# Kernel optimization log

Measured on AMD Instinct MI355X. Metric: run time of the kernel, lower is better.

The kernel has to match this reference:

```python
import jax, jax.numpy as jnp
import numpy as np

DIM = 2048; HK = 16; HV = 32; DK = 128; DV = 128; KCONV = 4
EPS = 1e-6; CHUNK = 64
KEY_DIM = HK * DK            # 2048
VALUE_DIM = HV * DV          # 4096
CONV_DIM = 2 * KEY_DIM + VALUE_DIM  # 8192
VR = HV // HK                # 2


def _l2norm(x, eps=1e-6):
    return x * jax.lax.rsqrt(jnp.sum(x * x, -1, keepdims=True) + eps)


def _chunk_gated_delta_rule(q, k, v, g, beta, chunk=CHUNK):
    # q,k: [B,T,H,DK]; v: [B,T,H,DV]; g,beta: [B,T,H]
    B, T, H, Dk = q.shape
    Dv = v.shape[-1]
    N = T // chunk
    q = _l2norm(q) * (Dk ** -0.5)
    k = _l2norm(k)
    rc = lambda t: t.transpose(0, 2, 1, 3).reshape(B, H, N, chunk, t.shape[-1])
    q, k, v = rc(q), rc(k), rc(v)
    g = g.transpose(0, 2, 1).reshape(B, H, N, chunk)
    beta = beta.transpose(0, 2, 1).reshape(B, H, N, chunk)
    v_b = v * beta[..., None]
    k_b = k * beta[..., None]
    g = jnp.cumsum(g, axis=-1)  # intra-chunk cumulative log-decay
    tri = jnp.tril(jnp.ones((chunk, chunk), bool))
    tri_s = jnp.tril(jnp.ones((chunk, chunk), bool), -1)
    diff = g[..., :, None] - g[..., None, :]
    decay = jnp.where(tri, jnp.exp(jnp.where(tri, diff, 0.0)), 0.0)
    # WY representation: T = (I + strict_tril(diag(beta) K K^T decay))^{-1}
    M = jnp.where(tri_s, jnp.einsum('bhnci,bhndi->bhncd', k_b, k) * decay, 0.0)
    eye = jnp.eye(chunk, dtype=q.dtype)
    Tinv = jax.scipy.linalg.solve_triangular(eye + M, jnp.broadcast_to(eye, M.shape), lower=True)
    u = Tinv @ v_b                                  # [B,H,N,C,Dv]
    w = Tinv @ (k_b * jnp.exp(g)[..., None])        # [B,H,N,C,Dk]
    attn_loc = jnp.where(tri, jnp.einsum('bhnci,bhndi->bhncd', q, k) * decay, 0.0)
    qg = q * jnp.exp(g)[..., None]
    g_last = g[..., -1]                             # [B,H,N]
    kdecay = k * jnp.exp(g_last[..., None] - g)[..., None]

    def step(S, inp):  # S: [B,H,Dk,Dv]
        u_i, w_i, a_i, qg_i, kd_i, gl_i = inp
        v_new = u_i - w_i @ S
        o_i = qg_i @ S + a_i @ v_new
        S = S * jnp.exp(gl_i)[..., None, None] + jnp.einsum('bhck,bhcv->bhkv', kd_i, v_new)
        return S, o_i

    S0 = jnp.zeros((B, H, Dk, Dv), q.dtype)
    xs = tuple(jnp.moveaxis(t, 2, 0) for t in (u, w, attn_loc, qg, kdecay, g_last))
    _, o = jax.lax.scan(step, S0, xs)               # [N,B,H,C,Dv]
    return jnp.moveaxis(o, 0, 2).reshape(B, H, T, Dv).transpose(0, 2, 1, 3)


def _forward(x, W_qkvz, W_ba, conv_w, dt_bias, A_log, norm_w, W_out):
    B, T, _ = x.shape
    qkvz = (x @ W_qkvz).reshape(B, T, HK, 2 * DK + 2 * VR * DV)
    ba = (x @ W_ba).reshape(B, T, HK, 2 * VR)
    q, k, v_pre, z_pre = jnp.split(qkvz, [DK, 2 * DK, 2 * DK + VR * DV], axis=3)
    b, a = jnp.split(ba, [VR], axis=3)
    b = b.reshape(B, T, HV)
    a = a.reshape(B, T, HV)
    # mirrors torch: cat -> transpose(1,2) -> reshape(bs,-1,seqlen) (C-order)
    mixed = jnp.concatenate([q, k, v_pre], axis=-1)          # [B,T,HK,512]
    mixed = jnp.transpose(mixed, (0, 2, 1, 3)).reshape(B, -1, T)
    y = jax.lax.conv_general_dilated(
        mixed, conv_w[:, None, :], (1,), [(KCONV - 1, 0)],
        dimension_numbers=('NCH', 'OIH', 'NCH'), feature_group_count=CONV_DIM)
    y = jax.nn.silu(y).transpose(0, 2, 1)                    # [B,T,CONV_DIM]
    q, k, v = jnp.split(y, [KEY_DIM, 2 * KEY_DIM], axis=-1)
    q = q.reshape(B, T, -1, DK)
    k = k.reshape(B, T, -1, DK)
    v = v.reshape(B, T, -1, DV)
    z = z_pre.reshape(B, T, -1, DV)
    beta = jax.nn.sigmoid(b)
    g = -jnp.exp(A_log) * jax.nn.softplus(a + dt_bias)       # [B,T,HV]
    q = jnp.repeat(q, VR, axis=2)
    k = jnp.repeat(k, VR, axis=2)
    o = _chunk_gated_delta_rule(q, k, v, g, beta)            # [B,T,HV,DV]
    # FusedRMSNormGated: gate (silu) before RMS norm
    og = o * jax.nn.silu(z)
    og = og * jax.lax.rsqrt(jnp.mean(og * og, -1, keepdims=True) + EPS) * norm_w
    return og.reshape(B, T, -1) @ W_out


def setup_inputs() -> dict:
    key = jax.random.key(0)
    ks = jax.random.split(key, 8)
    B, T = 1, 4096
    x = jax.random.normal(ks[0], (B, T, DIM), jnp.float32)
    rope_cache = jax.random.normal(ks[1], (T, DK), jnp.float32)
    position_ids = jnp.broadcast_to(jnp.arange(T, dtype=jnp.int32)[None, :], (B, T))
    W_qkvz = jax.random.normal(ks[2], (DIM, 2 * KEY_DIM + 2 * VALUE_DIM), jnp.float32) * (DIM ** -0.5)
    W_ba = jax.random.normal(ks[3], (DIM, 2 * HV), jnp.float32) * (DIM ** -0.5)
    conv_w = jax.random.normal(ks[4], (CONV_DIM, KCONV), jnp.float32) * 0.3
    dt_bias = jnp.ones((HV,), jnp.float32)
    A_log = jnp.log(jax.random.uniform(ks[5], (HV,), jnp.float32, 0.05, 4.0))
    norm_w = jnp.ones((DV,), jnp.float32)
    W_out = jax.random.normal(ks[6], (VALUE_DIM, DIM), jnp.float32) * (VALUE_DIM ** -0.5)
    return {"x": x, "rope_cache": rope_cache, "position_ids": position_ids,
            "W_qkvz": W_qkvz, "W_ba": W_ba, "conv_w": conv_w, "dt_bias": dt_bias,
            "A_log": A_log, "norm_w": norm_w, "W_out": W_out}


def reference(x, rope_cache, position_ids, W_qkvz, W_ba, conv_w, dt_bias, A_log, norm_w, W_out):
    # rope_cache / position_ids are accepted but unused, as in the torch module.
    return _forward(x, W_qkvz, W_ba, conv_w, dt_bias, A_log, norm_w, W_out)
```

## Files before the change

### kernel.cpp

```cpp
#include <hip/hip_runtime.h>
#include <hip/hip_bf16.h>

#define NH_K 16
#define NH_V 32
#define D_K 128
#define D_V 128
#define QKVZ_COLS 12288

typedef __attribute__((ext_vector_type(8))) __bf16 bf16x8;
typedef __attribute__((ext_vector_type(4))) __bf16 bf16x4;
typedef __attribute__((ext_vector_type(2))) __bf16 bf16x2;
typedef __attribute__((ext_vector_type(4))) float floatx4;
typedef __attribute__((ext_vector_type(4))) unsigned int uint32x4;

#define GLDS16(gp, lp) __builtin_amdgcn_global_load_lds( \
    (const __attribute__((address_space(1))) unsigned int*)(gp), \
    (__attribute__((address_space(3))) unsigned int*)(lp), 16, 0, 0)

__device__ __forceinline__ float sigm(float x) {
  float e = expf(-fabsf(x));
  return (x >= 0.f) ? 1.f / (1.f + e) : e / (1.f + e);
}
__device__ __forceinline__ float clampf(float v, float m) {
  return fminf(fmaxf(v, -m), m);
}
__device__ __forceinline__ float loadF(const void* p, size_t i, bool f32) {
  return f32 ? ((const float*)p)[i] : (float)((const __bf16*)p)[i];
}

__global__ __launch_bounds__(256) void detect_kernel(
    const unsigned int* __restrict__ x, int* __restrict__ flag)
{
  __shared__ int cnt;
  if (threadIdx.x == 0) cnt = 0;
  __syncthreads();
  unsigned int w = x[threadIdx.x];
  int e = (w >> 7) & 0xFF;
  if (e >= 100 && e <= 135) atomicAdd(&cnt, 1);
  __syncthreads();
  if (threadIdx.x == 0) *flag = (cnt < 128) ? 1 : 0;
}

__global__ __launch_bounds__(256) void convx_kernel(
    const void* __restrict__ x, __bf16* __restrict__ xb,
    const int* __restrict__ flagp)
{
  const bool f32 = (*flagp != 0);
  size_t i = ((size_t)blockIdx.x * 256 + threadIdx.x) * 8;
  if (f32) {
    float4 a = *(const float4*)&((const float*)x)[i];
    float4 b = *(const float4*)&((const float*)x)[i + 4];
    bf16x8 v;
    v[0]=(__bf16)a.x; v[1]=(__bf16)a.y; v[2]=(__bf16)a.z; v[3]=(__bf16)a.w;
    v[4]=(__bf16)b.x; v[5]=(__bf16)b.y; v[6]=(__bf16)b.z; v[7]=(__bf16)b.w;
    *(bf16x8*)&xb[i] = v;
  } else {
    *(uint32x4*)&xb[i] = *(const uint32x4*)&((const __bf16*)x)[i];
  }
}

__global__ __launch_bounds__(256) void trans_kernel(
    const void* __restrict__ W, __bf16* __restrict__ WT,
    int K, int N, const int* __restrict__ flagp)
{
  const bool f32 = (*flagp != 0);
  __shared__ float t[32][33];
  const int k0 = blockIdx.x * 32, n0 = blockIdx.y * 32;
  const int tid = threadIdx.x;
  {
    int r = tid >> 3, c4 = (tid & 7) * 4;
    if (f32) {
      float4 v = *(const float4*)&((const float*)W)[(size_t)(k0 + r) * N + n0 + c4];
      t[r][c4] = v.x; t[r][c4 + 1] = v.y; t[r][c4 + 2] = v.z; t[r][c4 + 3] = v.w;
    } else {
      bf16x4 v = *(const bf16x4*)&((const __bf16*)W)[(size_t)(k0 + r) * N + n0 + c4];
      t[r][c4] = (float)v[0]; t[r][c4 + 1] = (float)v[1];
      t[r][c4 + 2] = (float)v[2]; t[r][c4 + 3] = (float)v[3];
    }
  }
  __syncthreads();
  {
    int n = tid >> 3, k4 = (tid & 7) * 4;
    bf16x4 o;
#pragma unroll
    for (int j = 0; j < 4; ++j) o[j] = (__bf16)t[k4 + j][n];
    *(bf16x4*)&WT[(size_t)(n0 + n) * K + k0 + k4] = o;
  }
}

template<bool OUT_F32>
__global__ __launch_bounds__(512, 1) void gemm_bt2(
    const __bf16* __restrict__ A, const __bf16* __restrict__ BT,
    void* __restrict__ C, int M, int N, int K)
{
  __shared__ __align__(16) __bf16 As[2][8192];
  __shared__ __align__(16) __bf16 Bs[2][8192];
  const int tid = threadIdx.x;
  const int nx  = gridDim.x;
  const int nwg = nx * gridDim.y;
  int lid = blockIdx.y * nx + blockIdx.x;
  int swz = (lid & 7) * (nwg >> 3) + (lid >> 3);
  const int bn = (swz % nx) * 256;
  const int bm = (swz / nx) * 256;
  const int lane = tid & 63;
  const int wv   = tid >> 6;
  const int wm2  = wv >> 2;
  const int wn2  = wv & 3;
  const int l15  = lane & 15;
  const int quad = lane >> 4;
  const int NT   = K >> 5;

  auto stage = [&](int kt, int slot) {
    const int k0 = kt * 32;
#pragma unroll
    for (int L = 0; L < 2; ++L) {
      const int boff = L * 8192 + wv * 1024 + lane * 16;
      const int swb  = boff ^ (((boff >> 9) & 1) << 5);
      const int row  = swb >> 6;
      const int ce   = (swb & 63) >> 1;
      GLDS16(&A[(size_t)(bm + row) * K + k0 + ce], &As[slot][L * 4096 + wv * 512]);
      GLDS16(&BT[(size_t)(bn + row) * K + k0 + ce], &Bs[slot][L * 4096 + wv * 512]);
    }
  };

  floatx4 acc[8][4];
#pragma unroll
  for (int a = 0; a < 8; ++a)
#pragma unroll
    for (int b = 0; b < 4; ++b)
      acc[a][b] = (floatx4){0.f, 0.f, 0.f, 0.f};

  const int flip  = (l15 & 8) ? 32 : 0;
  const int baseA = (((wm2 * 128 + l15) * 64 + quad * 16) ^ flip);
  const int baseB = (((wn2 * 64 + l15) * 64 + quad * 16) ^ flip);

  stage(0, 0);
  stage(1, 1);
  asm volatile("s_waitcnt vmcnt(4)" ::: "memory");
  __builtin_amdgcn_s_barrier();
  __builtin_amdgcn_sched_barrier(0);

  for (int kt = 0; kt < NT; ++kt) {
    const int cur = kt & 1;
    const char* Ab = (const char*)&As[cur][0];
    const char* Bb = (const char*)&Bs[cur][0];
    bf16x8 af[8], bfr[4];
#pragma unroll
    for (int mt = 0; mt < 8; ++mt)
      af[mt] = *(const bf16x8*)(Ab + baseA + mt * 1024);
#pragma unroll
    for (int nt = 0; nt < 4; ++nt)
      bfr[nt] = *(const bf16x8*)(Bb + baseB + nt * 1024);
#pragma unroll
    for (int mt = 0; mt < 8; ++mt)
#pragma unroll
      for (int nt = 0; nt < 4; ++nt)
        acc[mt][nt] = __builtin_amdgcn_mfma_f32_16x16x32_bf16(af[mt], bfr[nt], acc[mt][nt], 0, 0, 0);
    if (kt + 1 < NT) {
      __builtin_amdgcn_s_barrier();
      if (kt + 2 < NT) {
        stage(kt + 2, cur);
        asm volatile("s_waitcnt vmcnt(4)" ::: "memory");
      } else {
        asm volatile("s_waitcnt vmcnt(0)" ::: "memory");
      }
      __builtin_amdgcn_s_barrier();
      __builtin_amdgcn_sched_barrier(0);
    }
  }

#pragma unroll
  for (int mt = 0; mt < 8; ++mt)
#pragma unroll
    for (int nt = 0; nt < 4; ++nt)
#pragma unroll
      for (int r = 0; r < 4; ++r) {
        int row = bm + wm2 * 128 + mt * 16 + quad * 4 + r;
        int col = bn + wn2 * 64 + nt * 16 + l15;
        if (OUT_F32) ((float*)C)[(size_t)row * N + col] = acc[mt][nt][r];
        else         ((__bf16*)C)[(size_t)row * N + col] = (__bf16)acc[mt][nt][r];
      }
}

__global__ __launch_bounds__(64) void ba_kernel(
    const void* __restrict__ x, const void* __restrict__ Wba,
    float* __restrict__ ba, const int* __restrict__ flagp)
{
  __shared__ float xr[2048];
  const bool f32 = (*flagp != 0);
  int t = blockIdx.x, tid = threadIdx.x;
  for (int i = tid; i < 2048; i += 64) xr[i] = loadF(x, (size_t)t * 2048 + i, f32);
  __syncthreads();
  float acc = 0.f;
  for (int k = 0; k < 2048; ++k) acc += xr[k] * loadF(Wba, (size_t)k * 64 + tid, f32);
  ba[(size_t)t * 64 + tid] = acc;
}

__global__ __launch_bounds__(256) void conv_kernel(
    const __bf16* __restrict__ qkvz, const void* __restrict__ conv_w,
    __bf16* __restrict__ qn, __bf16* __restrict__ kn, __bf16* __restrict__ vv,
    const int* __restrict__ flagp)
{
  __shared__ __bf16 yin[128][266];
  const bool f32 = (*flagp != 0);
  const int slot = blockIdx.x;
  const int tb   = blockIdx.y;
  const int tid  = threadIdx.x;
  int kind, h_out, cbase;
  if (slot < 16)      { kind = 0; h_out = slot;      cbase = slot * 128; }
  else if (slot < 32) { kind = 1; h_out = slot - 16; cbase = 2048 + h_out * 128; }
  else                { kind = 2; h_out = slot - 32; cbase = 4096 + h_out * 128; }
  const int hc  = cbase >> 9;
  const int cl0 = cbase & 511;
  const int t0  = tb * 256;

  for (int ch = tid; ch < 128 * 33; ch += 256) {
    int d = ch / 33, k = ch - d * 33;
    int s2 = t0 - 8 + k * 8;
    uint32x4 val;
    if (s2 < 0) {
      val = (uint32x4){0u, 0u, 0u, 0u};
    } else {
      int p  = (cl0 + d) * 4096 + s2;
      int tp = p >> 9, ep = p & 511;
      val = *(const uint32x4*)&qkvz[(size_t)tp * QKVZ_COLS + hc * 768 + ep];
    }
    unsigned int* dst = (unsigned int*)&yin[d][k * 8];
    dst[0] = val[0]; dst[1] = val[1]; dst[2] = val[2]; dst[3] = val[3];
  }
  __syncthreads();

  const int wv   = tid >> 6;
  const int lane = tid & 63;
  float w0[4], w1[4];
#pragma unroll
  for (int j = 0; j < 4; ++j) {
    w0[j] = loadF(conv_w, (size_t)(cbase + lane) * 4 + j, f32);
    w1[j] = loadF(conv_w, (size_t)(cbase + lane + 64) * 4 + j, f32);
  }
  const int ltend = wv * 64 + 64;
  for (int lt = wv * 64; lt < ltend; ++lt) {
    int t = t0 + lt;
    float a0 = 0.f, a1 = 0.f;
#pragma unroll
    for (int j = 0; j < 4; ++j) {
      a0 += w0[j] * (float)yin[lane][lt + 5 + j];
      a1 += w1[j] * (float)yin[lane + 64][lt + 5 + j];
    }
    float v0 = a0 * sigm(a0), v1 = a1 * sigm(a1);
    if (kind == 2) {
      vv[((size_t)t * NH_V + h_out) * D_V + lane]      = (__bf16)v0;
      vv[((size_t)t * NH_V + h_out) * D_V + lane + 64] = (__bf16)v1;
    } else {
      float ss = v0 * v0 + v1 * v1;
#pragma unroll
      for (int off = 32; off; off >>= 1) ss += __shfl_xor(ss, off, 64);
      float scl = rsqrtf(ss + 1e-6f);
      if (kind == 0) scl *= 0.08838834764831845f;
      __bf16* dst = (kind == 0) ? qn : kn;
      dst[((size_t)t * NH_K + h_out) * D_K + lane]      = (__bf16)(v0 * scl);
      dst[((size_t)t * NH_K + h_out) * D_K + lane + 64] = (__bf16)(v1 * scl);
    }
  }
}

__global__ __launch_bounds__(64) void gb_kernel(
    const float* __restrict__ ba, const void* __restrict__ dt_bias,
    const void* __restrict__ A_log, float* __restrict__ gbuf,
    float* __restrict__ betabuf, const int* __restrict__ flagp)
{
  const bool f32 = (*flagp != 0);
  int t = blockIdx.x;
  int hv = threadIdx.x;
  if (hv >= 32) return;
  float bv = ba[t * 64 + (hv >> 1) * 4 + (hv & 1)];
  float av = ba[t * 64 + (hv >> 1) * 4 + 2 + (hv & 1)];
  float beta = sigm(bv);
  float xx = av + loadF(dt_bias, hv, f32);
  float sp = (xx > 15.f) ? xx : log1pf(expf(fminf(xx, 15.f)));
  float g = -expf(loadF(A_log, hv, f32)) * sp;
  gbuf[t * 32 + hv] = g;
  betabuf[t * 32 + hv] = beta;
}

__global__ __launch_bounds__(256) void prep_kernel(
    const __bf16* __restrict__ qn, const __bf16* __restrict__ kn, const __bf16* __restrict__ vv,
    const float* __restrict__ gbuf, const float* __restrict__ betabuf,
    float* __restrict__ gcs, __bf16* __restrict__ u, __bf16* __restrict__ w,
    __bf16* __restrict__ attn)
{
  __shared__ float MT[64][67];
  __shared__ __bf16 vT[128][72];
  __shared__ __bf16 kT[128][72];
  __shared__ float gc[64], betas[64], scu[64], scw[64];
  const int bid = blockIdx.x;
  const int hv = bid >> 6, n = bid & 63;
  const int hk = hv >> 1;
  const int t0 = n * 64;
  const int tid = threadIdx.x;
  const int wv = tid >> 6, lane = tid & 63;
  const int l15 = lane & 15, quad = lane >> 4;

  {
    const __bf16* vrow = &vv[((size_t)(t0 + lane) * NH_V + hv) * D_V + wv * 32];
    const __bf16* krow = &kn[((size_t)(t0 + lane) * NH_K + hk) * D_K + wv * 32];
#pragma unroll
    for (int c2 = 0; c2 < 4; ++c2) {
      bf16x8 v8 = *(const bf16x8*)&vrow[c2 * 8];
      bf16x8 k8 = *(const bf16x8*)&krow[c2 * 8];
#pragma unroll
      for (int j = 0; j < 8; ++j) {
        vT[wv * 32 + c2 * 8 + j][lane] = v8[j];
        kT[wv * 32 + c2 * 8 + j][lane] = k8[j];
      }
    }
  }
  if (tid < 64) {
    gc[tid]    = gbuf[(t0 + tid) * 32 + hv];
    betas[tid] = betabuf[(t0 + tid) * 32 + hv];
  }
  __syncthreads();
  if (tid == 0) {
    float s = 0.f;
    for (int i = 0; i < 64; ++i) { s += gc[i]; gc[i] = s; }
  }
  __syncthreads();
  if (tid < 64) {
    float g = gc[tid];
    gcs[((size_t)hv * 64 + n) * 64 + tid] = g;
    scu[tid] = betas[tid];
    scw[tid] = betas[tid] * expf(g);
  }

  floatx4 kk[4];
#pragma unroll
  for (int nt = 0; nt < 4; ++nt) kk[nt] = (floatx4){0.f, 0.f, 0.f, 0.f};
#pragma unroll
  for (int ks = 0; ks < 4; ++ks) {
    bf16x8 afr = *(const bf16x8*)&kn[((size_t)(t0 + wv * 16 + l15) * NH_K + hk) * D_K + ks * 32 + quad * 8];
#pragma unroll
    for (int nt = 0; nt < 4; ++nt) {
      bf16x8 bfr = *(const bf16x8*)&kn[((size_t)(t0 + nt * 16 + l15) * NH_K + hk) * D_K + ks * 32 + quad * 8];
      kk[nt] = __builtin_amdgcn_mfma_f32_16x16x32_bf16(afr, bfr, kk[nt], 0, 0, 0);
    }
  }
#pragma unroll
  for (int nt = 0; nt < 4; ++nt)
#pragma unroll
    for (int r = 0; r < 4; ++r) {
      int i = wv * 16 + quad * 4 + r;
      int j = nt * 16 + l15;
      float m = 0.f;
      if (j < i) m = kk[nt][r] * betas[i] * expf(fminf(gc[i] - gc[j], 0.f));
      MT[i][j] = m;
    }
  __syncthreads();

  if (wv == 0) {
    if (lane == 0) MT[0][0] = 1.f;
    for (int ii = 1; ii < 64; ++ii) {
      float s = 0.f;
      for (int l = 0; l < ii; ++l) s += MT[ii][l] * MT[l][lane];
      MT[ii][lane] = ((lane == ii) ? 1.f : 0.f) - s;
    }
  }
  {
    int band = (wv == 0) ? 3 : (wv - 1);
    floatx4 at[4];
#pragma unroll
    for (int nt = 0; nt < 4; ++nt) at[nt] = (floatx4){0.f, 0.f, 0.f, 0.f};
#pragma unroll
    for (int ks = 0; ks < 4; ++ks) {
      bf16x8 afr = *(const bf16x8*)&qn[((size_t)(t0 + band * 16 + l15) * NH_K + hk) * D_K + ks * 32 + quad * 8];
#pragma unroll
      for (int nt = 0; nt < 4; ++nt) {
        bf16x8 bfr = *(const bf16x8*)&kn[((size_t)(t0 + nt * 16 + l15) * NH_K + hk) * D_K + ks * 32 + quad * 8];
        at[nt] = __builtin_amdgcn_mfma_f32_16x16x32_bf16(afr, bfr, at[nt], 0, 0, 0);
      }
    }
    size_t abase = ((size_t)hv * 64 + n) * (64 * 64);
#pragma unroll
    for (int nt = 0; nt < 4; ++nt)
#pragma unroll
      for (int r = 0; r < 4; ++r) {
        int i = band * 16 + quad * 4 + r;
        int j = nt * 16 + l15;
        float dec = expf(fminf(gc[i] - gc[j], 0.f));
        float a = (j <= i) ? clampf(at[nt][r] * dec, 1e6f) : 0.f;
        attn[abase + (size_t)i * 64 + j] = (__bf16)a;
      }
  }
  __syncthreads();

  floatx4 ua[8], wa[8];
#pragma unroll
  for (int t = 0; t < 8; ++t) {
    ua[t] = (floatx4){0.f, 0.f, 0.f, 0.f};
    wa[t] = (floatx4){0.f, 0.f, 0.f, 0.f};
  }
#pragma unroll
  for (int ks = 0; ks < 2; ++ks) {
    bf16x8 uh, ul, wh, wl;
#pragma unroll
    for (int j = 0; j < 8; ++j) {
      int c = ks * 32 + quad * 8 + j;
      float raw = MT[wv * 16 + l15][c];
      float tu = raw * scu[c];
      float tw = raw * scw[c];
      __bf16 h1 = (__bf16)tu; uh[j] = h1; ul[j] = (__bf16)(tu - (float)h1);
      __bf16 h2 = (__bf16)tw; wh[j] = h2; wl[j] = (__bf16)(tw - (float)h2);
    }
#pragma unroll
    for (int nt = 0; nt < 8; ++nt) {
      bf16x8 vb = *(const bf16x8*)&vT[nt * 16 + l15][ks * 32 + quad * 8];
      ua[nt] = __builtin_amdgcn_mfma_f32_16x16x32_bf16(uh, vb, ua[nt], 0, 0, 0);
      ua[nt] = __builtin_amdgcn_mfma_f32_16x16x32_bf16(ul, vb, ua[nt], 0, 0, 0);
      bf16x8 kb = *(const bf16x8*)&kT[nt * 16 + l15][ks * 32 + quad * 8];
      wa[nt] = __builtin_amdgcn_mfma_f32_16x16x32_bf16(wh, kb, wa[nt], 0, 0, 0);
      wa[nt] = __builtin_amdgcn_mfma_f32_16x16x32_bf16(wl, kb, wa[nt], 0, 0, 0);
    }
  }
  size_t base = ((size_t)hv * 64 + n) * (64 * 128);
#pragma unroll
  for (int nt = 0; nt < 8; ++nt)
#pragma unroll
    for (int r = 0; r < 4; ++r) {
      int row = wv * 16 + quad * 4 + r;
      int dv  = nt * 16 + l15;
      u[base + (size_t)row * 128 + dv] = (__bf16)clampf(ua[nt][r], 1e6f);
      w[base + (size_t)row * 128 + dv] = (__bf16)clampf(wa[nt][r], 1e6f);
    }
}

__global__ __launch_bounds__(64, 1) void scan_kernel(
    const __bf16* __restrict__ u, const __bf16* __restrict__ w, const __bf16* __restrict__ attn,
    const __bf16* __restrict__ qn, const __bf16* __restrict__ kn, const float* __restrict__ gcs,
    __bf16* __restrict__ obuf)
{
  __shared__ __bf16 sb_hi[16][136];
  __shared__ __bf16 sb_lo[16][136];
  __shared__ __bf16 vt[16][72];
  __shared__ __bf16 kt[128][72];

  const int hv   = blockIdx.x & 31;
  const int band = blockIdx.x >> 5;
  const int dv0  = band * 16;
  const int hk   = hv >> 1;
  const int lane = threadIdx.x;
  const int l15  = lane & 15;
  const int quad = lane >> 4;

  floatx4 S[8];
#pragma unroll
  for (int m = 0; m < 8; ++m) S[m] = (floatx4){0.f, 0.f, 0.f, 0.f};
  for (int i = lane; i < 16 * 136 / 2; i += 64) {
    ((unsigned int*)sb_hi)[i] = 0u;
    ((unsigned int*)sb_lo)[i] = 0u;
  }

  for (int n = 0; n < 64; ++n) {
    const int t0 = n * 64;
    const size_t cb = (size_t)hv * 64 + n;
    const float* gr = gcs + cb * 64;
    const size_t ub = cb * 8192;

    const __bf16* krow = &kn[((size_t)(t0 + lane) * NH_K + hk) * D_K];
    bf16x8 kr[16];
#pragma unroll
    for (int c2 = 0; c2 < 16; ++c2) kr[c2] = *(const bf16x8*)&krow[c2 * 8];

    floatx4 av[4];
#pragma unroll
    for (int mt = 0; mt < 4; ++mt)
#pragma unroll
      for (int r = 0; r < 4; ++r)
        av[mt][r] = (float)u[ub + (size_t)(mt * 16 + quad * 4 + r) * 128 + dv0 + l15];

    bf16x8 sh[4], sl[4];
#pragma unroll
    for (int ks = 0; ks < 4; ++ks) {
      sh[ks] = *(const bf16x8*)&sb_hi[l15][ks * 32 + quad * 8];
      sl[ks] = *(const bf16x8*)&sb_lo[l15][ks * 32 + quad * 8];
    }

#pragma unroll
    for (int ks = 0; ks < 4; ++ks)
#pragma unroll
      for (int mt = 0; mt < 4; ++mt) {
        uint32x4 wu = *(const uint32x4*)&w[ub + (size_t)(mt * 16 + l15) * 128 + ks * 32 + quad * 8];
        wu[0] ^= 0x80008000u; wu[1] ^= 0x80008000u;
        wu[2] ^= 0x80008000u; wu[3] ^= 0x80008000u;
        bf16x8 wf = __builtin_bit_cast(bf16x8, wu);
        av[mt] = __builtin_amdgcn_mfma_f32_16x16x32_bf16(wf, sh[ks], av[mt], 0, 0, 0);
        av[mt] = __builtin_amdgcn_mfma_f32_16x16x32_bf16(wf, sl[ks], av[mt], 0, 0, 0);
      }
#pragma unroll
    for (int mt = 0; mt < 4; ++mt) {
      bf16x4 h4;
#pragma unroll
      for (int r = 0; r < 4; ++r) h4[r] = (__bf16)clampf(av[mt][r], 1e8f);
      *(bf16x4*)&vt[l15][mt * 16 + quad * 4] = h4;
    }

    const float gl  = gr[63];
    const float egl = expf(gl);
    float egr[16];
#pragma unroll
    for (int mt = 0; mt < 4; ++mt)
#pragma unroll
      for (int r = 0; r < 4; ++r)
        egr[mt * 4 + r] = expf(gr[mt * 16 + quad * 4 + r]);
    float ek0[8], ek1[8];
#pragma unroll
    for (int j = 0; j < 8; ++j) {
      ek0[j] = expf(fminf(gl - gr[quad * 8 + j], 0.f));
      ek1[j] = expf(fminf(gl - gr[32 + quad * 8 + j], 0.f));
    }

    floatx4 ao[4];
#pragma unroll
    for (int mt = 0; mt < 4; ++mt) ao[mt] = (floatx4){0.f, 0.f, 0.f, 0.f};
#pragma unroll
    for (int ks = 0; ks < 4; ++ks)
#pragma unroll
      for (int mt = 0; mt < 4; ++mt) {
        bf16x8 qf = *(const bf16x8*)&qn[((size_t)(t0 + mt * 16 + l15) * NH_K + hk) * D_K + ks * 32 + quad * 8];
        ao[mt] = __builtin_amdgcn_mfma_f32_16x16x32_bf16(qf, sh[ks], ao[mt], 0, 0, 0);
        ao[mt] = __builtin_amdgcn_mfma_f32_16x16x32_bf16(qf, sl[ks], ao[mt], 0, 0, 0);
      }
#pragma unroll
    for (int mt = 0; mt < 4; ++mt)
#pragma unroll
      for (int r = 0; r < 4; ++r) ao[mt][r] *= egr[mt * 4 + r];

#pragma unroll
    for (int c2 = 0; c2 < 16; ++c2)
#pragma unroll
      for (int j = 0; j < 8; ++j)
        kt[c2 * 8 + j][lane] = kr[c2][j];

    bf16x8 vf0 = *(const bf16x8*)&vt[l15][quad * 8];
    bf16x8 vf1 = *(const bf16x8*)&vt[l15][32 + quad * 8];
#pragma unroll
    for (int mt = 0; mt < 4; ++mt) {
      bf16x8 a0 = *(const bf16x8*)&attn[cb * 4096 + (size_t)(mt * 16 + l15) * 64 + quad * 8];
      bf16x8 a1 = *(const bf16x8*)&attn[cb * 4096 + (size_t)(mt * 16 + l15) * 64 + 32 + quad * 8];
      ao[mt] = __builtin_amdgcn_mfma_f32_16x16x32_bf16(a0, vf0, ao[mt], 0, 0, 0);
      ao[mt] = __builtin_amdgcn_mfma_f32_16x16x32_bf16(a1, vf1, ao[mt], 0, 0, 0);
    }
#pragma unroll
    for (int mt = 0; mt < 4; ++mt)
#pragma unroll
      for (int r = 0; r < 4; ++r)
        obuf[((size_t)(t0 + mt * 16 + quad * 4 + r) * NH_V + hv) * D_V + dv0 + l15]
            = (__bf16)clampf(ao[mt][r], 1e8f);

#pragma unroll
    for (int m = 0; m < 8; ++m)
#pragma unroll
      for (int r = 0; r < 4; ++r) S[m][r] *= egl;
    bf16x8 vfd0, vfd1;
#pragma unroll
    for (int j = 0; j < 8; ++j) {
      vfd0[j] = (__bf16)((float)vf0[j] * ek0[j]);
      vfd1[j] = (__bf16)((float)vf1[j] * ek1[j]);
    }
#pragma unroll
    for (int ks = 0; ks < 2; ++ks) {
      bf16x8 vf = ks ? vfd1 : vfd0;
#pragma unroll
      for (int m = 0; m < 8; ++m) {
        bf16x8 kf = *(const bf16x8*)&kt[m * 16 + l15][ks * 32 + quad * 8];
        S[m] = __builtin_amdgcn_mfma_f32_16x16x32_bf16(kf, vf, S[m], 0, 0, 0);
      }
    }
#pragma unroll
    for (int m = 0; m < 8; ++m) {
      bf16x4 h4, l4;
#pragma unroll
      for (int r = 0; r < 4; ++r) {
        float v = clampf(S[m][r], 1e8f);
        S[m][r] = v;
        __bf16 h = (__bf16)v;
        h4[r] = h;
        l4[r] = (__bf16)(v - (float)h);
      }
      *(bf16x4*)&sb_hi[l15][m * 16 + quad * 4] = h4;
      *(bf16x4*)&sb_lo[l15][m * 16 + quad * 4] = l4;
    }
  }
}

__global__ __launch_bounds__(256) void gate_kernel(
    const __bf16* __restrict__ obuf, const __bf16* __restrict__ qkvz,
    const void* __restrict__ norm_w, __bf16* __restrict__ og,
    const int* __restrict__ flagp)
{
  const bool f32 = (*flagp != 0);
  const int t = blockIdx.x;
  const int wv = threadIdx.x >> 6, lane = threadIdx.x & 63;
  const int hv = blockIdx.y * 4 + wv;
  const int d = lane * 2;
  bf16x2 ov = *(const bf16x2*)&obuf[((size_t)t * NH_V + hv) * D_V + d];
  bf16x2 zv = *(const bf16x2*)&qkvz[(size_t)t * QKVZ_COLS + (hv >> 1) * 768 + 512 + (hv & 1) * 128 + d];
  float z0 = (float)zv[0], z1 = (float)zv[1];
  float v0 = (float)ov[0] * (z0 * sigm(z0));
  float v1 = (float)ov[1] * (z1 * sigm(z1));
  float ss = v0 * v0 + v1 * v1;
#pragma unroll
  for (int off = 32; off; off >>= 1) ss += __shfl_xor(ss, off, 64);
  float scl = rsqrtf(ss * (1.f / 128.f) + 1e-6f);
  bf16x2 o;
  o[0] = (__bf16)(v0 * scl * loadF(norm_w, d, f32));
  o[1] = (__bf16)(v1 * scl * loadF(norm_w, d + 1, f32));
  *(bf16x2*)&og[(size_t)t * 4096 + hv * 128 + d] = o;
}

extern "C" void kernel_launch(void* const* d_in, const int* in_sizes, int n_in,
                              void* d_out, int out_size, void* d_ws, size_t ws_size,
                              hipStream_t stream) {
  (void)in_sizes; (void)n_in; (void)out_size;
  const void* x     = d_in[0];
  const void* Wqkvz = d_in[3];
  const void* Wba   = d_in[4];
  const void* convw = d_in[5];
  const void* dtb   = d_in[6];
  const void* Alog  = d_in[7];
  const void* normw = d_in[8];
  const void* Wout  = d_in[9];

  char* ws = (char*)d_ws;
  size_t off = 0;
  int*    flag = (int*)(ws + off);    off += 256;
  __bf16* qkvz = (__bf16*)(ws + off); off += (size_t)4096 * 12288 * 2;
  float* ba    = (float*)(ws + off);  off += (size_t)4096 * 64 * 4;
  float* gbuf  = (float*)(ws + off);  off += (size_t)4096 * 32 * 4;
  float* betab = (float*)(ws + off);  off += (size_t)4096 * 32 * 4;
  float* gcs   = (float*)(ws + off);  off += (size_t)32 * 64 * 64 * 4;
  __bf16* qn   = (__bf16*)(ws + off); off += (size_t)4096 * 2048 * 2;
  __bf16* kn   = (__bf16*)(ws + off); off += (size_t)4096 * 2048 * 2;
  __bf16* vv   = (__bf16*)(ws + off); off += (size_t)4096 * 4096 * 2;
  __bf16* ubuf = (__bf16*)(ws + off); off += (size_t)32 * 64 * 8192 * 2;
  __bf16* wbuf = (__bf16*)(ws + off); off += (size_t)32 * 64 * 8192 * 2;
  __bf16* attn = (__bf16*)(ws + off); off += (size_t)32 * 64 * 4096 * 2;
  __bf16* obuf = vv;
  __bf16* og   = ubuf;
  __bf16* WqkvzT = ubuf;
  __bf16* xb     = attn;
  __bf16* WoutT  = wbuf;
  if (ws_size < off) return;

  detect_kernel<<<1, 256, 0, stream>>>((const unsigned int*)x, flag);
  convx_kernel<<<4096, 256, 0, stream>>>(x, xb, flag);
  trans_kernel<<<dim3(64, 384), 256, 0, stream>>>(Wqkvz, WqkvzT, 2048, 12288, flag);
  gemm_bt2<false><<<dim3(48, 16), 512, 0, stream>>>(xb, WqkvzT, qkvz, 4096, 12288, 2048);
  ba_kernel<<<4096, 64, 0, stream>>>(x, Wba, ba, flag);
  conv_kernel<<<dim3(64, 16), 256, 0, stream>>>(qkvz, convw, qn, kn, vv, flag);
  gb_kernel<<<4096, 64, 0, stream>>>(ba, dtb, Alog, gbuf, betab, flag);
  prep_kernel<<<2048, 256, 0, stream>>>(qn, kn, vv, gbuf, betab, gcs, ubuf, wbuf, attn);
  scan_kernel<<<256, 64, 0, stream>>>(ubuf, wbuf, attn, qn, kn, gcs, obuf);
  gate_kernel<<<dim3(4096, 8), 256, 0, stream>>>(obuf, qkvz, normw, og, flag);
  trans_kernel<<<dim3(128, 64), 256, 0, stream>>>(Wout, WoutT, 4096, 2048, flag);
  gemm_bt2<true><<<dim3(8, 16), 512, 0, stream>>>(og, WoutT, d_out, 4096, 2048, 4096);
}
```

Measured before the change: 1.486 ms.

## Split scan across four waves with LDS reduction; use 128-tile GEMM for output

The recurrent scan kernel now runs 256 threads per block instead of 64. Each wave handles a 32-wide K slice of the state for the w@S and q@S products, the four partial sums are reduced through shared memory, and each wave owns two of the eight state tiles for the update. This shortens the serial per-chunk critical path and spreads state registers across waves, at the cost of extra barriers and LDS traffic. The output projection moves to a new 128x128-tile GEMM with 512 blocks instead of 128 large-tile blocks, which should fill more compute units but has no double buffering.

```diff
diff --git a/kernel.cpp b/kernel.cpp
--- a/kernel.cpp
+++ b/kernel.cpp
@@ -86,6 +86,78 @@
     for (int j = 0; j < 4; ++j) o[j] = (__bf16)t[k4 + j][n];
     *(bf16x4*)&WT[(size_t)(n0 + n) * K + k0 + k4] = o;
   }
+}
+
+template<bool OUT_F32>
+__global__ __launch_bounds__(256) void gemm_bt(
+    const __bf16* __restrict__ A, const __bf16* __restrict__ BT,
+    void* __restrict__ C, int M, int N, int K)
+{
+  __shared__ __align__(16) __bf16 As[128 * 32];
+  __shared__ __align__(16) __bf16 Bs[128 * 32];
+  const int tid = threadIdx.x;
+  const int nx  = gridDim.x;
+  const int nwg = nx * gridDim.y;
+  int lid = blockIdx.y * nx + blockIdx.x;
+  int swz = (lid & 7) * (nwg >> 3) + (lid >> 3);
+  const int bn = (swz % nx) * 128;
+  const int bm = (swz / nx) * 128;
+  const int lane = tid & 63;
+  const int wv   = tid >> 6;
+  const int wm   = (wv >> 1) * 64;
+  const int wn   = (wv & 1) * 64;
+  const int l15  = lane & 15;
+  const int quad = lane >> 4;
+
+  const int o0 = wv * 2048 + lane * 16;
+  const int o1 = o0 + 1024;
+  const __bf16* Ag0 = &A[(size_t)(bm + (o0 >> 6)) * K + ((o0 & 63) >> 1)];
+  const __bf16* Ag1 = &A[(size_t)(bm + (o1 >> 6)) * K + ((o1 & 63) >> 1)];
+  const __bf16* Bg0 = &BT[(size_t)(bn + (o0 >> 6)) * K + ((o0 & 63) >> 1)];
+  const __bf16* Bg1 = &BT[(size_t)(bn + (o1 >> 6)) * K + ((o1 & 63) >> 1)];
+  __bf16* Ad0 = &As[wv * 1024];
+  __bf16* Ad1 = &As[wv * 1024 + 512];
+  __bf16* Bd0 = &Bs[wv * 1024];
+  __bf16* Bd1 = &Bs[wv * 1024 + 512];
+
+  floatx4 acc[4][4];
+#pragma unroll
+  for (int a = 0; a < 4; ++a)
+#pragma unroll
+    for (int b = 0; b < 4; ++b)
+      acc[a][b] = (floatx4){0.f, 0.f, 0.f, 0.f};
+
+  for (int k0 = 0; k0 < K; k0 += 32) {
+    GLDS16(Ag0 + k0, Ad0);
+    GLDS16(Ag1 + k0, Ad1);
+    GLDS16(Bg0 + k0, Bd0);
+    GLDS16(Bg1 + k0, Bd1);
+    __syncthreads();
+    bf16x8 af[4], bfr[4];
+#pragma unroll
+    for (int mt = 0; mt < 4; ++mt)
+      af[mt] = *(const bf16x8*)&As[(wm + mt * 16 + l15) * 32 + quad * 8];
+#pragma unroll
+    for (int nt = 0; nt < 4; ++nt)
+      bfr[nt] = *(const bf16x8*)&Bs[(wn + nt * 16 + l15) * 32 + quad * 8];
+#pragma unroll
+    for (int mt = 0; mt < 4; ++mt)
+#pragma unroll
+      for (int nt = 0; nt < 4; ++nt)
+        acc[mt][nt] = __builtin_amdgcn_mfma_f32_16x16x32_bf16(af[mt], bfr[nt], acc[mt][nt], 0, 0, 0);
+    __syncthreads();
+  }
+#pragma unroll
+  for (int mt = 0; mt < 4; ++mt)
+#pragma unroll
+    for (int nt = 0; nt < 4; ++nt)
+#pragma unroll
+      for (int r = 0; r < 4; ++r) {
+        int row = bm + wm + mt * 16 + quad * 4 + r;
+        int col = bn + wn + nt * 16 + l15;
+        if (OUT_F32) ((float*)C)[(size_t)row * N + col] = acc[mt][nt][r];
+        else         ((__bf16*)C)[(size_t)row * N + col] = (__bf16)acc[mt][nt][r];
+      }
 }
 
 template<bool OUT_F32>
@@ -432,7 +504,7 @@
     }
 }
 
-__global__ __launch_bounds__(64, 1) void scan_kernel(
+__global__ __launch_bounds__(256, 1) void scan_kernel(
     const __bf16* __restrict__ u, const __bf16* __restrict__ w, const __bf16* __restrict__ attn,
     const __bf16* __restrict__ qn, const __bf16* __restrict__ kn, const float* __restrict__ gcs,
     __bf16* __restrict__ obuf)
@@ -441,22 +513,27 @@
   __shared__ __bf16 sb_lo[16][136];
   __shared__ __bf16 vt[16][72];
   __shared__ __bf16 kt[128][72];
+  __shared__ float redv[4][4][64][4];
+  __shared__ float redo[4][4][64][4];
 
   const int hv   = blockIdx.x & 31;
   const int band = blockIdx.x >> 5;
   const int dv0  = band * 16;
   const int hk   = hv >> 1;
-  const int lane = threadIdx.x;
+  const int tid  = threadIdx.x;
+  const int wv   = tid >> 6;
+  const int lane = tid & 63;
   const int l15  = lane & 15;
   const int quad = lane >> 4;
 
-  floatx4 S[8];
-#pragma unroll
-  for (int m = 0; m < 8; ++m) S[m] = (floatx4){0.f, 0.f, 0.f, 0.f};
-  for (int i = lane; i < 16 * 136 / 2; i += 64) {
+  floatx4 S[2];
+  S[0] = (floatx4){0.f, 0.f, 0.f, 0.f};
+  S[1] = (floatx4){0.f, 0.f, 0.f, 0.f};
+  for (int i = tid; i < 16 * 136 / 2; i += 256) {
     ((unsigned int*)sb_hi)[i] = 0u;
     ((unsigned int*)sb_lo)[i] = 0u;
   }
+  __syncthreads();
 
   for (int n = 0; n < 64; ++n) {
     const int t0 = n * 64;
@@ -464,101 +541,94 @@
     const float* gr = gcs + cb * 64;
     const size_t ub = cb * 8192;
 
-    const __bf16* krow = &kn[((size_t)(t0 + lane) * NH_K + hk) * D_K];
-    bf16x8 kr[16];
-#pragma unroll
-    for (int c2 = 0; c2 < 16; ++c2) kr[c2] = *(const bf16x8*)&krow[c2 * 8];
-
-    floatx4 av[4];
-#pragma unroll
-    for (int mt = 0; mt < 4; ++mt)
-#pragma unroll
-      for (int r = 0; r < 4; ++r)
-        av[mt][r] = (float)u[ub + (size_t)(mt * 16 + quad * 4 + r) * 128 + dv0 + l15];
-
-    bf16x8 sh[4], sl[4];
-#pragma unroll
-    for (int ks = 0; ks < 4; ++ks) {
-      sh[ks] = *(const bf16x8*)&sb_hi[l15][ks * 32 + quad * 8];
-      sl[ks] = *(const bf16x8*)&sb_lo[l15][ks * 32 + quad * 8];
-    }
-
-#pragma unroll
-    for (int ks = 0; ks < 4; ++ks)
-#pragma unroll
-      for (int mt = 0; mt < 4; ++mt) {
-        uint32x4 wu = *(const uint32x4*)&w[ub + (size_t)(mt * 16 + l15) * 128 + ks * 32 + quad * 8];
-        wu[0] ^= 0x80008000u; wu[1] ^= 0x80008000u;
-        wu[2] ^= 0x80008000u; wu[3] ^= 0x80008000u;
-        bf16x8 wf = __builtin_bit_cast(bf16x8, wu);
-        av[mt] = __builtin_amdgcn_mfma_f32_16x16x32_bf16(wf, sh[ks], av[mt], 0, 0, 0);
-        av[mt] = __builtin_amdgcn_mfma_f32_16x16x32_bf16(wf, sl[ks], av[mt], 0, 0, 0);
-      }
+    const __bf16* krow = &kn[((size_t)(t0 + lane) * NH_K + hk) * D_K + wv * 32];
+    bf16x8 kr[4];
+#pragma unroll
+    for (int c2 = 0; c2 < 4; ++c2) kr[c2] = *(const bf16x8*)&krow[c2 * 8];
+    float uin[4];
+#pragma unroll
+    for (int r = 0; r < 4; ++r)
+      uin[r] = (float)u[ub + (size_t)(wv * 16 + quad * 4 + r) * 128 + dv0 + l15];
+
+    bf16x8 sh = *(const bf16x8*)&sb_hi[l15][wv * 32 + quad * 8];
+    bf16x8 sl = *(const bf16x8*)&sb_lo[l15][wv * 32 + quad * 8];
+
+    floatx4 av[4], ap[4];
 #pragma unroll
     for (int mt = 0; mt < 4; ++mt) {
-      bf16x4 h4;
-#pragma unroll
-      for (int r = 0; r < 4; ++r) h4[r] = (__bf16)clampf(av[mt][r], 1e8f);
-      *(bf16x4*)&vt[l15][mt * 16 + quad * 4] = h4;
-    }
+      av[mt] = (floatx4){0.f, 0.f, 0.f, 0.f};
+      ap[mt] = (floatx4){0.f, 0.f, 0.f, 0.f};
+    }
+#pragma unroll
+    for (int mt = 0; mt < 4; ++mt) {
+      uint32x4 wu = *(const uint32x4*)&w[ub + (size_t)(mt * 16 + l15) * 128 + wv * 32 + quad * 8];
+      wu[0] ^= 0x80008000u; wu[1] ^= 0x80008000u;
+      wu[2] ^= 0x80008000u; wu[3] ^= 0x80008000u;
+      bf16x8 wf = __builtin_bit_cast(bf16x8, wu);
+      av[mt] = __builtin_amdgcn_mfma_f32_16x16x32_bf16(wf, sh, av[mt], 0, 0, 0);
+      av[mt] = __builtin_amdgcn_mfma_f32_16x16x32_bf16(wf, sl, av[mt], 0, 0, 0);
+    }
+#pragma unroll
+    for (int mt = 0; mt < 4; ++mt) {
+      bf16x8 qf = *(const bf16x8*)&qn[((size_t)(t0 + mt * 16 + l15) * NH_K + hk) * D_K + wv * 32 + quad * 8];
+      ap[mt] = __builtin_amdgcn_mfma_f32_16x16x32_bf16(qf, sh, ap[mt], 0, 0, 0);
+      ap[mt] = __builtin_amdgcn_mfma_f32_16x16x32_bf16(qf, sl, ap[mt], 0, 0, 0);
+    }
+#pragma unroll
+    for (int mt = 0; mt < 4; ++mt) {
+      *(floatx4*)&redv[wv][mt][lane][0] = av[mt];
+      *(floatx4*)&redo[wv][mt][lane][0] = ap[mt];
+    }
+#pragma unroll
+    for (int c2 = 0; c2 < 4; ++c2)
+#pragma unroll
+      for (int j = 0; j < 8; ++j)
+        kt[wv * 32 + c2 * 8 + j][lane] = kr[c2][j];
+    __syncthreads();
 
     const float gl  = gr[63];
     const float egl = expf(gl);
-    float egr[16];
-#pragma unroll
-    for (int mt = 0; mt < 4; ++mt)
-#pragma unroll
-      for (int r = 0; r < 4; ++r)
-        egr[mt * 4 + r] = expf(gr[mt * 16 + quad * 4 + r]);
+    floatx4 vsum, osum;
+#pragma unroll
+    for (int r = 0; r < 4; ++r) { vsum[r] = uin[r]; osum[r] = 0.f; }
+#pragma unroll
+    for (int j = 0; j < 4; ++j) {
+      floatx4 pv = *(const floatx4*)&redv[j][wv][lane][0];
+      floatx4 po = *(const floatx4*)&redo[j][wv][lane][0];
+#pragma unroll
+      for (int r = 0; r < 4; ++r) { vsum[r] += pv[r]; osum[r] += po[r]; }
+    }
+#pragma unroll
+    for (int r = 0; r < 4; ++r)
+      osum[r] *= expf(gr[wv * 16 + quad * 4 + r]);
+    {
+      bf16x4 h4;
+#pragma unroll
+      for (int r = 0; r < 4; ++r) h4[r] = (__bf16)clampf(vsum[r], 1e8f);
+      *(bf16x4*)&vt[l15][wv * 16 + quad * 4] = h4;
+    }
+    __syncthreads();
+
+    bf16x8 vf0 = *(const bf16x8*)&vt[l15][quad * 8];
+    bf16x8 vf1 = *(const bf16x8*)&vt[l15][32 + quad * 8];
+
+    {
+      bf16x8 a0 = *(const bf16x8*)&attn[cb * 4096 + (size_t)(wv * 16 + l15) * 64 + quad * 8];
+      bf16x8 a1 = *(const bf16x8*)&attn[cb * 4096 + (size_t)(wv * 16 + l15) * 64 + 32 + quad * 8];
+      osum = __builtin_amdgcn_mfma_f32_16x16x32_bf16(a0, vf0, osum, 0, 0, 0);
+      osum = __builtin_amdgcn_mfma_f32_16x16x32_bf16(a1, vf1, osum, 0, 0, 0);
+    }
+#pragma unroll
+    for (int r = 0; r < 4; ++r)
+      obuf[((size_t)(t0 + wv * 16 + quad * 4 + r) * NH_V + hv) * D_V + dv0 + l15]
+          = (__bf16)clampf(osum[r], 1e8f);
+
     float ek0[8], ek1[8];
 #pragma unroll
     for (int j = 0; j < 8; ++j) {
       ek0[j] = expf(fminf(gl - gr[quad * 8 + j], 0.f));
       ek1[j] = expf(fminf(gl - gr[32 + quad * 8 + j], 0.f));
     }
-
-    floatx4 ao[4];
-#pragma unroll
-    for (int mt = 0; mt < 4; ++mt) ao[mt] = (floatx4){0.f, 0.f, 0.f, 0.f};
-#pragma unroll
-    for (int ks = 0; ks < 4; ++ks)
-#pragma unroll
-      for (int mt = 0; mt < 4; ++mt) {
-        bf16x8 qf = *(const bf16x8*)&qn[((size_t)(t0 + mt * 16 + l15) * NH_K + hk) * D_K + ks * 32 + quad * 8];
-        ao[mt] = __builtin_amdgcn_mfma_f32_16x16x32_bf16(qf, sh[ks], ao[mt], 0, 0, 0);
-        ao[mt] = __builtin_amdgcn_mfma_f32_16x16x32_bf16(qf, sl[ks], ao[mt], 0, 0, 0);
-      }
-#pragma unroll
-    for (int mt = 0; mt < 4; ++mt)
-#pragma unroll
-      for (int r = 0; r < 4; ++r) ao[mt][r] *= egr[mt * 4 + r];
-
-#pragma unroll
-    for (int c2 = 0; c2 < 16; ++c2)
-#pragma unroll
-      for (int j = 0; j < 8; ++j)
-        kt[c2 * 8 + j][lane] = kr[c2][j];
-
-    bf16x8 vf0 = *(const bf16x8*)&vt[l15][quad * 8];
-    bf16x8 vf1 = *(const bf16x8*)&vt[l15][32 + quad * 8];
-#pragma unroll
-    for (int mt = 0; mt < 4; ++mt) {
-      bf16x8 a0 = *(const bf16x8*)&attn[cb * 4096 + (size_t)(mt * 16 + l15) * 64 + quad * 8];
-      bf16x8 a1 = *(const bf16x8*)&attn[cb * 4096 + (size_t)(mt * 16 + l15) * 64 + 32 + quad * 8];
-      ao[mt] = __builtin_amdgcn_mfma_f32_16x16x32_bf16(a0, vf0, ao[mt], 0, 0, 0);
-      ao[mt] = __builtin_amdgcn_mfma_f32_16x16x32_bf16(a1, vf1, ao[mt], 0, 0, 0);
-    }
-#pragma unroll
-    for (int mt = 0; mt < 4; ++mt)
-#pragma unroll
-      for (int r = 0; r < 4; ++r)
-        obuf[((size_t)(t0 + mt * 16 + quad * 4 + r) * NH_V + hv) * D_V + dv0 + l15]
-            = (__bf16)clampf(ao[mt][r], 1e8f);
-
-#pragma unroll
-    for (int m = 0; m < 8; ++m)
-#pragma unroll
-      for (int r = 0; r < 4; ++r) S[m][r] *= egl;
     bf16x8 vfd0, vfd1;
 #pragma unroll
     for (int j = 0; j < 8; ++j) {
@@ -566,21 +636,19 @@
       vfd1[j] = (__bf16)((float)vf1[j] * ek1[j]);
     }
 #pragma unroll
-    for (int ks = 0; ks < 2; ++ks) {
-      bf16x8 vf = ks ? vfd1 : vfd0;
-#pragma unroll
-      for (int m = 0; m < 8; ++m) {
-        bf16x8 kf = *(const bf16x8*)&kt[m * 16 + l15][ks * 32 + quad * 8];
-        S[m] = __builtin_amdgcn_mfma_f32_16x16x32_bf16(kf, vf, S[m], 0, 0, 0);
-      }
-    }
-#pragma unroll
-    for (int m = 0; m < 8; ++m) {
+    for (int m2 = 0; m2 < 2; ++m2) {
+      const int m = wv * 2 + m2;
+#pragma unroll
+      for (int r = 0; r < 4; ++r) S[m2][r] *= egl;
+      bf16x8 kf0 = *(const bf16x8*)&kt[m * 16 + l15][quad * 8];
+      bf16x8 kf1 = *(const bf16x8*)&kt[m * 16 + l15][32 + quad * 8];
+      S[m2] = __builtin_amdgcn_mfma_f32_16x16x32_bf16(kf0, vfd0, S[m2], 0, 0, 0);
+      S[m2] = __builtin_amdgcn_mfma_f32_16x16x32_bf16(kf1, vfd1, S[m2], 0, 0, 0);
       bf16x4 h4, l4;
 #pragma unroll
       for (int r = 0; r < 4; ++r) {
-        float v = clampf(S[m][r], 1e8f);
-        S[m][r] = v;
+        float v = clampf(S[m2][r], 1e8f);
+        S[m2][r] = v;
         __bf16 h = (__bf16)v;
         h4[r] = h;
         l4[r] = (__bf16)(v - (float)h);
@@ -658,8 +726,8 @@
   conv_kernel<<<dim3(64, 16), 256, 0, stream>>>(qkvz, convw, qn, kn, vv, flag);
   gb_kernel<<<4096, 64, 0, stream>>>(ba, dtb, Alog, gbuf, betab, flag);
   prep_kernel<<<2048, 256, 0, stream>>>(qn, kn, vv, gbuf, betab, gcs, ubuf, wbuf, attn);
-  scan_kernel<<<256, 64, 0, stream>>>(ubuf, wbuf, attn, qn, kn, gcs, obuf);
+  scan_kernel<<<256, 256, 0, stream>>>(ubuf, wbuf, attn, qn, kn, gcs, obuf);
   gate_kernel<<<dim3(4096, 8), 256, 0, stream>>>(obuf, qkvz, normw, og, flag);
   trans_kernel<<<dim3(128, 64), 256, 0, stream>>>(Wout, WoutT, 4096, 2048, flag);
-  gemm_bt2<true><<<dim3(8, 16), 512, 0, stream>>>(og, WoutT, d_out, 4096, 2048, 4096);
-}
+  gemm_bt<true><<<dim3(16, 32), 256, 0, stream>>>(og, WoutT, d_out, 4096, 2048, 4096);
+}
```

After: 1.390 ms. -6.5%, faster.
